# Kernel tuning notes

Hardware: AMD Instinct MI355X
Metric: run time of the kernel (lower is better)

The kernel has to match this reference:

```python
import jax, jax.numpy as jnp
import numpy as np

B, S, D, H = 2, 2048, 1024, 16
HD = D // H  # head_dim = 64
ROPE_BASE = 10000.0
NEG_MIN = jnp.finfo(jnp.float32).min


def _rope_cos_sin(seq_len, head_dim):
    inv_freq = 1.0 / (ROPE_BASE ** (jnp.arange(0, head_dim, 2, dtype=jnp.float32) / head_dim))
    t = jnp.arange(seq_len, dtype=jnp.float32)
    freqs = jnp.einsum('i,j->ij', t, inv_freq)           # [S, HD/2]
    emb = jnp.concatenate([freqs, freqs], axis=-1)        # [S, HD]
    return jnp.cos(emb), jnp.sin(emb)


def _rotate_half(x):
    x1, x2 = jnp.split(x, 2, axis=-1)
    return jnp.concatenate([-x2, x1], axis=-1)


def setup_inputs() -> dict:
    key = jax.random.key(0)
    ks = jax.random.split(key, 5)
    sc = 0.02
    hidden_states = jax.random.normal(ks[0], (B, S, D), dtype=jnp.float32)
    wq = jax.random.normal(ks[1], (D, D), dtype=jnp.float32) * sc
    wk = jax.random.normal(ks[2], (D, D), dtype=jnp.float32) * sc
    wv = jax.random.normal(ks[3], (D, D), dtype=jnp.float32) * sc
    wo = jax.random.normal(ks[4], (D, D), dtype=jnp.float32) * sc
    # additive causal mask [B,1,S,S]: 0 on/below diagonal, large negative above
    causal = jnp.tril(jnp.ones((S, S), dtype=jnp.bool_))
    attention_mask = jnp.where(causal, 0.0, NEG_MIN)[None, None, :, :].astype(jnp.float32)
    attention_mask = jnp.broadcast_to(attention_mask, (B, 1, S, S))
    position_ids = jnp.broadcast_to(jnp.arange(S, dtype=jnp.int32)[None, :], (B, S))
    return {"hidden_states": hidden_states, "attention_mask": attention_mask,
            "wq": wq, "wk": wk, "wv": wv, "wo": wo, "position_ids": position_ids}


def reference(hidden_states, attention_mask, wq, wk, wv, wo, position_ids):
    bsz, q_len, _ = hidden_states.shape

    def shape_heads(x):
        return x.reshape(bsz, q_len, H, HD).transpose(0, 2, 1, 3)  # [B,H,S,HD]

    q = shape_heads(hidden_states @ wq)
    k = shape_heads(hidden_states @ wk)
    v = shape_heads(hidden_states @ wv)

    cos, sin = _rope_cos_sin(q_len, HD)                   # [S, HD]
    cos = cos[position_ids][:, None, :, :]                # [B,1,S,HD]
    sin = sin[position_ids][:, None, :, :]
    q = q * cos + _rotate_half(q) * sin
    k = k * cos + _rotate_half(k) * sin

    scores = jnp.einsum('bhqd,bhkd->bhqk', q, k) / jnp.sqrt(jnp.float32(HD))
    scores = jnp.maximum(scores + attention_mask, NEG_MIN)
    attn = jax.nn.softmax(scores, axis=-1)
    out = jnp.einsum('bhqk,bhkd->bhqd', attn, v)          # [B,H,S,HD]
    out = out.transpose(0, 2, 1, 3).reshape(bsz, q_len, D)
    return out @ wo
```

## Files before the change

kernel.cpp:

```cpp
#include <hip/hip_runtime.h>

#define B_ 2
#define S_ 2048
#define D_ 1024
#define H_ 16
#define HD_ 64

typedef unsigned short u16;
typedef __attribute__((ext_vector_type(8))) short short8;
typedef __attribute__((ext_vector_type(4))) float f32x4;

__device__ __forceinline__ u16 f2bf(float f) {
  union { float f; unsigned u; } v; v.f = f;
  unsigned r = v.u + 0x7fffu + ((v.u >> 16) & 1u);
  return (u16)(r >> 16);
}
__device__ __forceinline__ float bf2f(u16 b) {
  union { unsigned u; float f; } v; v.u = ((unsigned)b) << 16;
  return v.f;
}
__device__ __forceinline__ unsigned pkbf(float a, float b) {
  return (unsigned)f2bf(a) | ((unsigned)f2bf(b) << 16);
}
__device__ __forceinline__ void gload_lds16(const u16* g, u16* l) {
  __builtin_amdgcn_global_load_lds((const __attribute__((address_space(1))) void*)g,
                                   (__attribute__((address_space(3))) void*)l, 16, 0, 0);
}

__global__ __launch_bounds__(256) void cvt_kernel(const float* __restrict__ in,
                                                  u16* __restrict__ out, int n4) {
  int i = blockIdx.x * 256 + threadIdx.x;
  if (i >= n4) return;
  const float4 v = ((const float4*)in)[i];
  ushort4 o;
  o.x = f2bf(v.x); o.y = f2bf(v.y); o.z = f2bf(v.z); o.w = f2bf(v.w);
  ((ushort4*)out)[i] = o;
}

__global__ __launch_bounds__(256) void wtrans_kernel(const float* __restrict__ W0,
                                                     const float* __restrict__ W1,
                                                     const float* __restrict__ W2,
                                                     const float* __restrict__ W3,
                                                     u16* __restrict__ WT) {
  __shared__ float T[64][65];
  const float* Wz[4] = {W0, W1, W2, W3};
  const float* W = Wz[blockIdx.z];
  u16* dst = WT + (size_t)blockIdx.z * (1024 * 1024);
  const int nb = blockIdx.x * 64, kb = blockIdx.y * 64;
  const int t = threadIdx.x;
  const int r = t >> 2, c4 = (t & 3) * 16;
#pragma unroll
  for (int i = 0; i < 4; ++i) {
    float4 v = *(const float4*)&W[(kb + r) * D_ + nb + c4 + i * 4];
    T[r][c4 + i * 4 + 0] = v.x;
    T[r][c4 + i * 4 + 1] = v.y;
    T[r][c4 + i * 4 + 2] = v.z;
    T[r][c4 + i * 4 + 3] = v.w;
  }
  __syncthreads();
#pragma unroll
  for (int i = 0; i < 4; ++i) {
    ushort4 o;
    o.x = f2bf(T[c4 + i * 4 + 0][r]);
    o.y = f2bf(T[c4 + i * 4 + 1][r]);
    o.z = f2bf(T[c4 + i * 4 + 2][r]);
    o.w = f2bf(T[c4 + i * 4 + 3][r]);
    *(ushort4*)&dst[(nb + r) * D_ + kb + c4 + i * 4] = o;
  }
}

template <int BN, int MODE>
__global__ __launch_bounds__(256) void gemm_kernel(const u16* __restrict__ A,
                                                   const u16* __restrict__ BT,
                                                   float* __restrict__ out0,
                                                   u16* __restrict__ oQ,
                                                   u16* __restrict__ oK,
                                                   u16* __restrict__ oV,
                                                   const int* __restrict__ posarr) {
  constexpr int K = D_;
  constexpr int NT = BN / 32;
  constexpr int BI = BN / 32;
  __shared__ u16 As[128 * 64];
  __shared__ u16 Bs[BN * 64];
  const int t = threadIdx.x, lane = t & 63, w = t >> 6;
  const int l15 = lane & 15, quad = lane >> 4;
  const int n0 = blockIdx.x * BN, m0 = blockIdx.y * 128;
  const int wm = (w >> 1) * 64, wn = (w & 1) * (BN / 2);

  f32x4 acc[4][NT];
#pragma unroll
  for (int mt = 0; mt < 4; ++mt)
#pragma unroll
    for (int nt = 0; nt < NT; ++nt) acc[mt][nt] = (f32x4){0.f, 0.f, 0.f, 0.f};

  const u16* ag[4]; u16* al[4];
  const u16* bg[4]; u16* bl[4];
#pragma unroll
  for (int j = 0; j < 4; ++j) {
    int slot = w * 256 + j * 64 + lane;
    int row = slot >> 3, q = (slot & 7) ^ (row & 7);
    ag[j] = A + (size_t)(m0 + row) * K + q * 8;
    al[j] = (u16*)As + (size_t)(w * 256 + j * 64) * 8;
  }
#pragma unroll
  for (int j = 0; j < BI; ++j) {
    int slot = w * (BI * 64) + j * 64 + lane;
    int row = slot >> 3, q = (slot & 7) ^ (row & 7);
    bg[j] = BT + (size_t)(n0 + row) * K + q * 8;
    bl[j] = (u16*)Bs + (size_t)(w * (BI * 64) + j * 64) * 8;
  }

  for (int k0 = 0; k0 < K; k0 += 64) {
    __syncthreads();
#pragma unroll
    for (int j = 0; j < 4; ++j) gload_lds16(ag[j] + k0, al[j]);
#pragma unroll
    for (int j = 0; j < BI; ++j) gload_lds16(bg[j] + k0, bl[j]);
    __syncthreads();
#pragma unroll
    for (int kc = 0; kc < 2; ++kc) {
      short8 af[4], bf[NT];
#pragma unroll
      for (int mt = 0; mt < 4; ++mt) {
        int row = wm + mt * 16 + l15;
        af[mt] = *(const short8*)&As[row * 64 + (((kc * 4 + quad) ^ (row & 7)) * 8)];
      }
#pragma unroll
      for (int nt = 0; nt < NT; ++nt) {
        int col = wn + nt * 16 + l15;
        bf[nt] = *(const short8*)&Bs[col * 64 + (((kc * 4 + quad) ^ (col & 7)) * 8)];
      }
#pragma unroll
      for (int mt = 0; mt < 4; ++mt)
#pragma unroll
        for (int nt = 0; nt < NT; ++nt)
          acc[mt][nt] = __builtin_amdgcn_mfma_f32_16x16x32_bf16(af[mt], bf[nt], acc[mt][nt], 0, 0, 0);
    }
  }

  if (MODE == 0) {
#pragma unroll
    for (int mt = 0; mt < 4; ++mt) {
      const int row0 = m0 + wm + mt * 16 + quad * 4;
#pragma unroll
      for (int nt = 0; nt < NT; ++nt) {
        const int col = n0 + wn + nt * 16 + l15;
#pragma unroll
        for (int r = 0; r < 4; ++r) out0[(size_t)(row0 + r) * 1024 + col] = acc[mt][nt][r];
      }
    }
  } else {
    const int widx = n0 >> 10;
    if (widx == 2) {
#pragma unroll
      for (int mt = 0; mt < 4; ++mt) {
        const int row0 = m0 + wm + mt * 16 + quad * 4;
#pragma unroll
        for (int nt = 0; nt < NT; ++nt) {
          const int cc = (n0 + wn + nt * 16 + l15) & 1023;
          const int h = cc >> 6, d = cc & 63;
#pragma unroll
          for (int r = 0; r < 4; ++r) {
            const int rw = row0 + r;
            const int b = rw >> 11, s = rw & (S_ - 1);
            oV[(((size_t)(b * H_ + h) * HD_ + d) << 11) + s] = f2bf(acc[mt][nt][r]);
          }
        }
      }
    } else {
      u16* dst = (widx == 0) ? oQ : oK;
      const float scale = (widx == 0) ? 0.125f : 1.0f;
      float invf[2];
      invf[0] = exp2f(-0.41524101186f * (float)l15);
      invf[1] = exp2f(-0.41524101186f * (float)(16 + l15));
      const int h = ((n0 + wn) & 1023) >> 6;
#pragma unroll
      for (int mt = 0; mt < 4; ++mt) {
        const int row0 = m0 + wm + mt * 16 + quad * 4;
#pragma unroll
        for (int r = 0; r < 4; ++r) {
          const int rw = row0 + r;
          const int b = rw >> 11, s = rw & (S_ - 1);
          const float pos = (float)posarr[b * S_ + s];
          const size_t base = (((size_t)(b * H_ + h) * S_ + s) << 6);
#pragma unroll
          for (int nt2 = 0; nt2 < 2; ++nt2) {
            float sn, c;
            __sincosf(pos * invf[nt2], &sn, &c);
            const float x1 = acc[mt][nt2][r], x2 = acc[mt][nt2 + 2][r];
            const int d = nt2 * 16 + l15;
            dst[base + d] = f2bf((x1 * c - x2 * sn) * scale);
            dst[base + d + 32] = f2bf((x2 * c + x1 * sn) * scale);
          }
        }
      }
    }
  }
}

__global__ __launch_bounds__(256, 2) void attn_kernel(const u16* __restrict__ Q,
                                                      const u16* __restrict__ Kx,
                                                      const u16* __restrict__ Vt,
                                                      u16* __restrict__ AO) {
  __shared__ u16 Ks[2][512 * 8];
  __shared__ u16 Vs[2][512 * 8];
  __shared__ u16 Pw[4][128 * 8];
  const int t = threadIdx.x;
  const int lane = t & 63, w = t >> 6;
  const int l15 = lane & 15, quad = lane >> 4;
  const int idx = blockIdx.x;
  const int pr = (idx >> 3) & 15;
  const int bh = (idx & 7) | ((idx >> 7) << 3);
  const int qtA = pr, qtB = 31 - pr;
  const u16* qp = Q + bh * (S_ * HD_);
  const u16* kp = Kx + bh * (S_ * HD_);
  const u16* vp = Vt + bh * (HD_ * S_);
  const int wq16 = w * 16;
  const int q_loA = qtA * 64 + wq16;
  const int q_loB = qtB * 64 + wq16;

  int srow[2], sq[2];
#pragma unroll
  for (int jj = 0; jj < 2; ++jj) {
    int slot = w * 128 + jj * 64 + lane;
    srow[jj] = slot >> 3;
    sq[jj] = (slot & 7) ^ (srow[jj] & 7);
  }
  auto stage = [&](int kt, int buf) {
#pragma unroll
    for (int jj = 0; jj < 2; ++jj)
      gload_lds16(kp + (size_t)(kt * 64 + srow[jj]) * 64 + sq[jj] * 8,
                  &Ks[buf][(w * 128 + jj * 64) * 8]);
#pragma unroll
    for (int jj = 0; jj < 2; ++jj)
      gload_lds16(vp + (size_t)srow[jj] * S_ + kt * 64 + sq[jj] * 8,
                  &Vs[buf][(w * 128 + jj * 64) * 8]);
  };

  short8 qfA[2], qfB[2];
#pragma unroll
  for (int kc = 0; kc < 2; ++kc) {
    qfA[kc] = *(const short8*)&qp[(q_loA + l15) * HD_ + kc * 32 + quad * 8];
    qfB[kc] = *(const short8*)&qp[(q_loB + l15) * HD_ + kc * 32 + quad * 8];
  }

  f32x4 oA[4], oB[4];
  float mA = -INFINITY, lA = 0.f, mB = -INFINITY, lB = 0.f;
#pragma unroll
  for (int i = 0; i < 4; ++i) {
    oA[i] = (f32x4){0.f, 0.f, 0.f, 0.f};
    oB[i] = (f32x4){0.f, 0.f, 0.f, 0.f};
  }

  auto chainStep = [&](bool diag, const short8* qf, const short8* kf, const short8* vf,
                       f32x4* o, float& m_, float& l_) {
    f32x4 sa[4];
#pragma unroll
    for (int i = 0; i < 4; ++i) sa[i] = (f32x4){0.f, 0.f, 0.f, 0.f};
#pragma unroll
    for (int kc = 0; kc < 2; ++kc)
#pragma unroll
      for (int nt = 0; nt < 4; ++nt)
        sa[nt] = __builtin_amdgcn_mfma_f32_16x16x32_bf16(kf[kc * 4 + nt], qf[kc], sa[nt], 0, 0, 0);
    if (diag) {
#pragma unroll
      for (int nt = 0; nt < 4; ++nt)
#pragma unroll
        for (int r = 0; r < 4; ++r)
          if (nt * 16 + quad * 4 + r > wq16 + l15) sa[nt][r] = -INFINITY;
    }
    float mx = -INFINITY;
#pragma unroll
    for (int nt = 0; nt < 4; ++nt)
#pragma unroll
      for (int r = 0; r < 4; ++r) mx = fmaxf(mx, sa[nt][r]);
    mx = fmaxf(mx, __shfl_xor(mx, 16));
    mx = fmaxf(mx, __shfl_xor(mx, 32));
    const float mn = fmaxf(m_, mx);
    const float alpha = __expf(m_ - mn);
    m_ = mn;
    float p[16];
    float sum = 0.f;
#pragma unroll
    for (int nt = 0; nt < 4; ++nt)
#pragma unroll
      for (int r = 0; r < 4; ++r) {
        const float pe = __expf(sa[nt][r] - mn);
        p[nt * 4 + r] = pe;
        sum += pe;
      }
    sum += __shfl_xor(sum, 16);
    sum += __shfl_xor(sum, 32);
    l_ = l_ * alpha + sum;
#pragma unroll
    for (int dt = 0; dt < 4; ++dt)
#pragma unroll
      for (int r = 0; r < 4; ++r) o[dt][r] *= alpha;
#pragma unroll
    for (int nt = 0; nt < 4; ++nt) {
      const int q = nt * 2 + (quad >> 1);
      uint2 pk;
      pk.x = pkbf(p[nt * 4 + 0], p[nt * 4 + 1]);
      pk.y = pkbf(p[nt * 4 + 2], p[nt * 4 + 3]);
      *(uint2*)&Pw[w][(l15 * 8 + (q ^ (l15 & 7))) * 8 + (quad & 1) * 4] = pk;
    }
#pragma unroll
    for (int kc = 0; kc < 2; ++kc) {
      short8 pf = *(const short8*)&Pw[w][(l15 * 8 + (((kc * 4) + quad) ^ (l15 & 7))) * 8];
#pragma unroll
      for (int dt = 0; dt < 4; ++dt)
        o[dt] = __builtin_amdgcn_mfma_f32_16x16x32_bf16(vf[dt * 2 + kc], pf, o[dt], 0, 0, 0);
    }
  };

  const int ktmax = qtB;
  stage(0, 0);
  int kt = 0;
  while (true) {
    __syncthreads();
    if (kt < ktmax) stage(kt + 1, (kt + 1) & 1);
    const int buf = kt & 1;
    short8 kf[8], vf[8];
#pragma unroll
    for (int kc = 0; kc < 2; ++kc)
#pragma unroll
      for (int nt = 0; nt < 4; ++nt) {
        const int row = nt * 16 + l15;
        kf[kc * 4 + nt] =
            *(const short8*)&Ks[buf][(row * 8 + ((kc * 4 + quad) ^ (row & 7))) * 8];
      }
#pragma unroll
    for (int dt = 0; dt < 4; ++dt)
#pragma unroll
      for (int kc = 0; kc < 2; ++kc) {
        const int row = dt * 16 + l15;
        vf[dt * 2 + kc] =
            *(const short8*)&Vs[buf][(row * 8 + ((kc * 4 + quad) ^ (row & 7))) * 8];
      }
    chainStep(kt == qtB, qfB, kf, vf, oB, mB, lB);
    if (kt <= qtA) chainStep(kt == qtA, qfA, kf, vf, oA, mA, lA);
    if (++kt > ktmax) break;
  }

  const int b = bh >> 4, h = bh & 15;
  const float liA = 1.0f / lA, liB = 1.0f / lB;
  const size_t baseA = ((size_t)(b * S_ + q_loA + l15)) * D_ + h * HD_;
  const size_t baseB = ((size_t)(b * S_ + q_loB + l15)) * D_ + h * HD_;
#pragma unroll
  for (int dt = 0; dt < 4; ++dt)
#pragma unroll
    for (int rr = 0; rr < 2; ++rr) {
      *(unsigned*)&AO[baseA + dt * 16 + quad * 4 + rr * 2] =
          pkbf(oA[dt][rr * 2] * liA, oA[dt][rr * 2 + 1] * liA);
      *(unsigned*)&AO[baseB + dt * 16 + quad * 4 + rr * 2] =
          pkbf(oB[dt][rr * 2] * liB, oB[dt][rr * 2 + 1] * liB);
    }
}

extern "C" void kernel_launch(void* const* d_in, const int* in_sizes, int n_in,
                              void* d_out, int out_size, void* d_ws, size_t ws_size,
                              hipStream_t stream) {
  const float* hs = (const float*)d_in[0];
  const float* wq = (const float*)d_in[2];
  const float* wk = (const float*)d_in[3];
  const float* wv = (const float*)d_in[4];
  const float* wo = (const float*)d_in[5];
  const int* pos = (const int*)d_in[6];
  float* out = (float*)d_out;

  char* ws = (char*)d_ws;
  const size_t MB = (size_t)1 << 20;
  u16* Xb = (u16*)(ws);
  u16* WT = (u16*)(ws + 8 * MB);
  u16* Qh = (u16*)(ws + 16 * MB);
  u16* Kh = (u16*)(ws + 24 * MB);
  u16* Vt = (u16*)(ws + 32 * MB);
  u16* AO = (u16*)(ws + 40 * MB);

  cvt_kernel<<<(B_ * S_ * D_) / 4 / 256, 256, 0, stream>>>(hs, Xb, (B_ * S_ * D_) / 4);
  wtrans_kernel<<<dim3(16, 16, 4), 256, 0, stream>>>(wq, wk, wv, wo, WT);

  gemm_kernel<128, 1><<<dim3(24, 32), 256, 0, stream>>>(Xb, WT, nullptr, Qh, Kh, Vt, pos);

  attn_kernel<<<512, 256, 0, stream>>>(Qh, Kh, Vt, AO);

  gemm_kernel<64, 0><<<dim3(16, 32), 256, 0, stream>>>(AO, WT + 3 * 1024 * 1024, out,
                                                       nullptr, nullptr, nullptr, nullptr);
}
```

Measured before the change: 214.3 us.

## Fuse prep kernels, restructure attention scheduling, double-buffer output GEMM, stage V epilogue

Merges the activation cast and weight transpose into one prep launch. Attention now runs one query tile per block over 1024 blocks, with heavier tiles scheduled first and occupancy raised to 4 blocks per CU, replacing the paired light/heavy tiles. The output projection uses a double-buffered LDS pipeline with 128-wide N tiles. The V-transpose epilogue stages results through LDS so the global stores are coalesced. These changes trade load balancing for more parallelism and add LDS usage and register-pressure risk.

```diff
diff --git a/kernel.cpp b/kernel.cpp
--- a/kernel.cpp
+++ b/kernel.cpp
@@ -27,22 +27,26 @@
                                    (__attribute__((address_space(3))) void*)l, 16, 0, 0);
 }
 
-__global__ __launch_bounds__(256) void cvt_kernel(const float* __restrict__ in,
-                                                  u16* __restrict__ out, int n4) {
-  int i = blockIdx.x * 256 + threadIdx.x;
-  if (i >= n4) return;
-  const float4 v = ((const float4*)in)[i];
-  ushort4 o;
-  o.x = f2bf(v.x); o.y = f2bf(v.y); o.z = f2bf(v.z); o.w = f2bf(v.w);
-  ((ushort4*)out)[i] = o;
-}
-
-__global__ __launch_bounds__(256) void wtrans_kernel(const float* __restrict__ W0,
-                                                     const float* __restrict__ W1,
-                                                     const float* __restrict__ W2,
-                                                     const float* __restrict__ W3,
-                                                     u16* __restrict__ WT) {
+__global__ __launch_bounds__(256) void prep_kernel(const float* __restrict__ hs,
+                                                   const float* __restrict__ W0,
+                                                   const float* __restrict__ W1,
+                                                   const float* __restrict__ W2,
+                                                   const float* __restrict__ W3,
+                                                   u16* __restrict__ Xb,
+                                                   u16* __restrict__ WT) {
   __shared__ float T[64][65];
+  if (blockIdx.z == 4) {
+    const int base = (blockIdx.y * 16 + blockIdx.x) * 4096 + threadIdx.x;
+#pragma unroll 4
+    for (int i = 0; i < 16; ++i) {
+      const int idx = base + i * 256;
+      const float4 v = ((const float4*)hs)[idx];
+      ushort4 o;
+      o.x = f2bf(v.x); o.y = f2bf(v.y); o.z = f2bf(v.z); o.w = f2bf(v.w);
+      ((ushort4*)Xb)[idx] = o;
+    }
+    return;
+  }
   const float* Wz[4] = {W0, W1, W2, W3};
   const float* W = Wz[blockIdx.z];
   u16* dst = WT + (size_t)blockIdx.z * (1024 * 1024);
@@ -69,7 +73,7 @@
   }
 }
 
-template <int BN, int MODE>
+template <int BN, int MODE, int DB>
 __global__ __launch_bounds__(256) void gemm_kernel(const u16* __restrict__ A,
                                                    const u16* __restrict__ BT,
                                                    float* __restrict__ out0,
@@ -80,8 +84,15 @@
   constexpr int K = D_;
   constexpr int NT = BN / 32;
   constexpr int BI = BN / 32;
-  __shared__ u16 As[128 * 64];
-  __shared__ u16 Bs[BN * 64];
+  constexpr int ABANK = 128 * 64;
+  constexpr int BBANK = BN * 64;
+  constexpr int STAGE = (DB + 1) * (ABANK + BBANK);
+  constexpr int EPIU = (MODE == 1) ? 128 * 136 : 0;
+  constexpr int SMU = STAGE > EPIU ? STAGE : EPIU;
+  __shared__ u16 smem[SMU];
+  u16* AsP = smem;
+  u16* BsP = smem + (DB + 1) * ABANK;
+
   const int t = threadIdx.x, lane = t & 63, w = t >> 6;
   const int l15 = lane & 15, quad = lane >> 4;
   const int n0 = blockIdx.x * BN, m0 = blockIdx.y * 128;
@@ -93,48 +104,67 @@
 #pragma unroll
     for (int nt = 0; nt < NT; ++nt) acc[mt][nt] = (f32x4){0.f, 0.f, 0.f, 0.f};
 
-  const u16* ag[4]; u16* al[4];
-  const u16* bg[4]; u16* bl[4];
+  const u16* ag[4]; int aoff[4];
+  const u16* bg[BI]; int boff[BI];
 #pragma unroll
   for (int j = 0; j < 4; ++j) {
     int slot = w * 256 + j * 64 + lane;
     int row = slot >> 3, q = (slot & 7) ^ (row & 7);
     ag[j] = A + (size_t)(m0 + row) * K + q * 8;
-    al[j] = (u16*)As + (size_t)(w * 256 + j * 64) * 8;
+    aoff[j] = (w * 256 + j * 64) * 8;
   }
 #pragma unroll
   for (int j = 0; j < BI; ++j) {
     int slot = w * (BI * 64) + j * 64 + lane;
     int row = slot >> 3, q = (slot & 7) ^ (row & 7);
     bg[j] = BT + (size_t)(n0 + row) * K + q * 8;
-    bl[j] = (u16*)Bs + (size_t)(w * (BI * 64) + j * 64) * 8;
-  }
-
-  for (int k0 = 0; k0 < K; k0 += 64) {
-    __syncthreads();
-#pragma unroll
-    for (int j = 0; j < 4; ++j) gload_lds16(ag[j] + k0, al[j]);
-#pragma unroll
-    for (int j = 0; j < BI; ++j) gload_lds16(bg[j] + k0, bl[j]);
-    __syncthreads();
+    boff[j] = (w * (BI * 64) + j * 64) * 8;
+  }
+
+  auto stage = [&](int k0, int buf) {
+#pragma unroll
+    for (int j = 0; j < 4; ++j) gload_lds16(ag[j] + k0, AsP + buf * ABANK + aoff[j]);
+#pragma unroll
+    for (int j = 0; j < BI; ++j) gload_lds16(bg[j] + k0, BsP + buf * BBANK + boff[j]);
+  };
+  auto compute = [&](int buf) {
+    const u16* Ab = AsP + buf * ABANK;
+    const u16* Bb = BsP + buf * BBANK;
 #pragma unroll
     for (int kc = 0; kc < 2; ++kc) {
       short8 af[4], bf[NT];
 #pragma unroll
       for (int mt = 0; mt < 4; ++mt) {
         int row = wm + mt * 16 + l15;
-        af[mt] = *(const short8*)&As[row * 64 + (((kc * 4 + quad) ^ (row & 7)) * 8)];
+        af[mt] = *(const short8*)&Ab[row * 64 + (((kc * 4 + quad) ^ (row & 7)) * 8)];
       }
 #pragma unroll
       for (int nt = 0; nt < NT; ++nt) {
         int col = wn + nt * 16 + l15;
-        bf[nt] = *(const short8*)&Bs[col * 64 + (((kc * 4 + quad) ^ (col & 7)) * 8)];
+        bf[nt] = *(const short8*)&Bb[col * 64 + (((kc * 4 + quad) ^ (col & 7)) * 8)];
       }
 #pragma unroll
       for (int mt = 0; mt < 4; ++mt)
 #pragma unroll
         for (int nt = 0; nt < NT; ++nt)
           acc[mt][nt] = __builtin_amdgcn_mfma_f32_16x16x32_bf16(af[mt], bf[nt], acc[mt][nt], 0, 0, 0);
+    }
+  };
+
+  if constexpr (DB == 0) {
+    for (int k0 = 0; k0 < K; k0 += 64) {
+      __syncthreads();
+      stage(k0, 0);
+      __syncthreads();
+      compute(0);
+    }
+  } else {
+    stage(0, 0);
+#pragma unroll 1
+    for (int it = 0; it < K / 64; ++it) {
+      __syncthreads();
+      if (it + 1 < K / 64) stage((it + 1) * 64, (it + 1) & 1);
+      compute(it & 1);
     }
   }
 
@@ -152,21 +182,30 @@
   } else {
     const int widx = n0 >> 10;
     if (widx == 2) {
-#pragma unroll
-      for (int mt = 0; mt < 4; ++mt) {
-        const int row0 = m0 + wm + mt * 16 + quad * 4;
-#pragma unroll
-        for (int nt = 0; nt < NT; ++nt) {
-          const int cc = (n0 + wn + nt * 16 + l15) & 1023;
-          const int h = cc >> 6, d = cc & 63;
-#pragma unroll
-          for (int r = 0; r < 4; ++r) {
-            const int rw = row0 + r;
-            const int b = rw >> 11, s = rw & (S_ - 1);
-            oV[(((size_t)(b * H_ + h) * HD_ + d) << 11) + s] = f2bf(acc[mt][nt][r]);
-          }
+      __syncthreads();
+      u16* Epi = smem;
+#pragma unroll
+      for (int nt = 0; nt < NT; ++nt) {
+        const int col = wn + nt * 16 + l15;
+#pragma unroll
+        for (int mt = 0; mt < 4; ++mt) {
+          const int row0 = wm + mt * 16 + quad * 4;
+          uint2 pk;
+          pk.x = pkbf(acc[mt][nt][0], acc[mt][nt][1]);
+          pk.y = pkbf(acc[mt][nt][2], acc[mt][nt][3]);
+          *(uint2*)&Epi[col * 136 + row0] = pk;
         }
       }
+      __syncthreads();
+      const int col = t >> 1, half = t & 1;
+      const int cc = (n0 + col) & 1023;
+      const int h = cc >> 6, d = cc & 63;
+      const int bb = m0 >> 11;
+      const int s0 = (m0 & (S_ - 1)) + half * 64;
+      u16* gp = oV + ((((size_t)(bb * H_ + h) * HD_ + d)) << 11) + s0;
+#pragma unroll
+      for (int i = 0; i < 8; ++i)
+        ((uint4*)gp)[i] = *(const uint4*)&Epi[col * 136 + half * 64 + i * 8];
     } else {
       u16* dst = (widx == 0) ? oQ : oK;
       const float scale = (widx == 0) ? 0.125f : 1.0f;
@@ -198,7 +237,7 @@
   }
 }
 
-__global__ __launch_bounds__(256, 2) void attn_kernel(const u16* __restrict__ Q,
+__global__ __launch_bounds__(256, 4) void attn_kernel(const u16* __restrict__ Q,
                                                       const u16* __restrict__ Kx,
                                                       const u16* __restrict__ Vt,
                                                       u16* __restrict__ AO) {
@@ -209,15 +248,13 @@
   const int lane = t & 63, w = t >> 6;
   const int l15 = lane & 15, quad = lane >> 4;
   const int idx = blockIdx.x;
-  const int pr = (idx >> 3) & 15;
-  const int bh = (idx & 7) | ((idx >> 7) << 3);
-  const int qtA = pr, qtB = 31 - pr;
+  const int bh = (idx & 7) | ((idx >> 8) << 3);
+  const int qt = 31 - ((idx >> 3) & 31);
   const u16* qp = Q + bh * (S_ * HD_);
   const u16* kp = Kx + bh * (S_ * HD_);
   const u16* vp = Vt + bh * (HD_ * S_);
   const int wq16 = w * 16;
-  const int q_loA = qtA * 64 + wq16;
-  const int q_loB = qtB * 64 + wq16;
+  const int q_lo = qt * 64 + wq16;
 
   int srow[2], sq[2];
 #pragma unroll
@@ -237,23 +274,38 @@
                   &Vs[buf][(w * 128 + jj * 64) * 8]);
   };
 
-  short8 qfA[2], qfB[2];
-#pragma unroll
-  for (int kc = 0; kc < 2; ++kc) {
-    qfA[kc] = *(const short8*)&qp[(q_loA + l15) * HD_ + kc * 32 + quad * 8];
-    qfB[kc] = *(const short8*)&qp[(q_loB + l15) * HD_ + kc * 32 + quad * 8];
-  }
-
-  f32x4 oA[4], oB[4];
-  float mA = -INFINITY, lA = 0.f, mB = -INFINITY, lB = 0.f;
-#pragma unroll
-  for (int i = 0; i < 4; ++i) {
-    oA[i] = (f32x4){0.f, 0.f, 0.f, 0.f};
-    oB[i] = (f32x4){0.f, 0.f, 0.f, 0.f};
-  }
-
-  auto chainStep = [&](bool diag, const short8* qf, const short8* kf, const short8* vf,
-                       f32x4* o, float& m_, float& l_) {
+  short8 qf[2];
+#pragma unroll
+  for (int kc = 0; kc < 2; ++kc)
+    qf[kc] = *(const short8*)&qp[(q_lo + l15) * HD_ + kc * 32 + quad * 8];
+
+  f32x4 o[4];
+  float m_ = -INFINITY, l_ = 0.f;
+#pragma unroll
+  for (int i = 0; i < 4; ++i) o[i] = (f32x4){0.f, 0.f, 0.f, 0.f};
+
+  stage(0, 0);
+  for (int kt = 0; kt <= qt; ++kt) {
+    __syncthreads();
+    if (kt < qt) stage(kt + 1, (kt + 1) & 1);
+    const int buf = kt & 1;
+    short8 kf[8], vf[8];
+#pragma unroll
+    for (int kc = 0; kc < 2; ++kc)
+#pragma unroll
+      for (int nt = 0; nt < 4; ++nt) {
+        const int row = nt * 16 + l15;
+        kf[kc * 4 + nt] =
+            *(const short8*)&Ks[buf][(row * 8 + ((kc * 4 + quad) ^ (row & 7))) * 8];
+      }
+#pragma unroll
+    for (int dt = 0; dt < 4; ++dt)
+#pragma unroll
+      for (int kc = 0; kc < 2; ++kc) {
+        const int row = dt * 16 + l15;
+        vf[dt * 2 + kc] =
+            *(const short8*)&Vs[buf][(row * 8 + ((kc * 4 + quad) ^ (row & 7))) * 8];
+      }
     f32x4 sa[4];
 #pragma unroll
     for (int i = 0; i < 4; ++i) sa[i] = (f32x4){0.f, 0.f, 0.f, 0.f};
@@ -262,7 +314,7 @@
 #pragma unroll
       for (int nt = 0; nt < 4; ++nt)
         sa[nt] = __builtin_amdgcn_mfma_f32_16x16x32_bf16(kf[kc * 4 + nt], qf[kc], sa[nt], 0, 0, 0);
-    if (diag) {
+    if (kt == qt) {
 #pragma unroll
       for (int nt = 0; nt < 4; ++nt)
 #pragma unroll
@@ -311,50 +363,17 @@
       for (int dt = 0; dt < 4; ++dt)
         o[dt] = __builtin_amdgcn_mfma_f32_16x16x32_bf16(vf[dt * 2 + kc], pf, o[dt], 0, 0, 0);
     }
-  };
-
-  const int ktmax = qtB;
-  stage(0, 0);
-  int kt = 0;
-  while (true) {
-    __syncthreads();
-    if (kt < ktmax) stage(kt + 1, (kt + 1) & 1);
-    const int buf = kt & 1;
-    short8 kf[8], vf[8];
-#pragma unroll
-    for (int kc = 0; kc < 2; ++kc)
-#pragma unroll
-      for (int nt = 0; nt < 4; ++nt) {
-        const int row = nt * 16 + l15;
-        kf[kc * 4 + nt] =
-            *(const short8*)&Ks[buf][(row * 8 + ((kc * 4 + quad) ^ (row & 7))) * 8];
-      }
-#pragma unroll
-    for (int dt = 0; dt < 4; ++dt)
-#pragma unroll
-      for (int kc = 0; kc < 2; ++kc) {
-        const int row = dt * 16 + l15;
-        vf[dt * 2 + kc] =
-            *(const short8*)&Vs[buf][(row * 8 + ((kc * 4 + quad) ^ (row & 7))) * 8];
-      }
-    chainStep(kt == qtB, qfB, kf, vf, oB, mB, lB);
-    if (kt <= qtA) chainStep(kt == qtA, qfA, kf, vf, oA, mA, lA);
-    if (++kt > ktmax) break;
   }
 
   const int b = bh >> 4, h = bh & 15;
-  const float liA = 1.0f / lA, liB = 1.0f / lB;
-  const size_t baseA = ((size_t)(b * S_ + q_loA + l15)) * D_ + h * HD_;
-  const size_t baseB = ((size_t)(b * S_ + q_loB + l15)) * D_ + h * HD_;
+  const float li = 1.0f / l_;
+  const size_t base = ((size_t)(b * S_ + q_lo + l15)) * D_ + h * HD_;
 #pragma unroll
   for (int dt = 0; dt < 4; ++dt)
 #pragma unroll
-    for (int rr = 0; rr < 2; ++rr) {
-      *(unsigned*)&AO[baseA + dt * 16 + quad * 4 + rr * 2] =
-          pkbf(oA[dt][rr * 2] * liA, oA[dt][rr * 2 + 1] * liA);
-      *(unsigned*)&AO[baseB + dt * 16 + quad * 4 + rr * 2] =
-          pkbf(oB[dt][rr * 2] * liB, oB[dt][rr * 2 + 1] * liB);
-    }
+    for (int rr = 0; rr < 2; ++rr)
+      *(unsigned*)&AO[base + dt * 16 + quad * 4 + rr * 2] =
+          pkbf(o[dt][rr * 2] * li, o[dt][rr * 2 + 1] * li);
 }
 
 extern "C" void kernel_launch(void* const* d_in, const int* in_sizes, int n_in,
@@ -377,13 +396,12 @@
   u16* Vt = (u16*)(ws + 32 * MB);
   u16* AO = (u16*)(ws + 40 * MB);
 
-  cvt_kernel<<<(B_ * S_ * D_) / 4 / 256, 256, 0, stream>>>(hs, Xb, (B_ * S_ * D_) / 4);
-  wtrans_kernel<<<dim3(16, 16, 4), 256, 0, stream>>>(wq, wk, wv, wo, WT);
-
-  gemm_kernel<128, 1><<<dim3(24, 32), 256, 0, stream>>>(Xb, WT, nullptr, Qh, Kh, Vt, pos);
-
-  attn_kernel<<<512, 256, 0, stream>>>(Qh, Kh, Vt, AO);
-
-  gemm_kernel<64, 0><<<dim3(16, 32), 256, 0, stream>>>(AO, WT + 3 * 1024 * 1024, out,
-                                                       nullptr, nullptr, nullptr, nullptr);
-}
+  prep_kernel<<<dim3(16, 16, 5), 256, 0, stream>>>(hs, wq, wk, wv, wo, Xb, WT);
+
+  gemm_kernel<128, 1, 0><<<dim3(24, 32), 256, 0, stream>>>(Xb, WT, nullptr, Qh, Kh, Vt, pos);
+
+  attn_kernel<<<1024, 256, 0, stream>>>(Qh, Kh, Vt, AO);
+
+  gemm_kernel<128, 0, 1><<<dim3(8, 32), 256, 0, stream>>>(AO, WT + 3 * 1024 * 1024, out,
+                                                          nullptr, nullptr, nullptr, nullptr);
+}
```

Measured after the change: 231.6 us. 8.1% more time.
